# Kernel tuning notes

Measured on AMD Instinct MI355X. Metric: run time of the kernel, lower is better.

## Reference

```python
import jax, jax.numpy as jnp
import numpy as np
from math import sqrt

D_MODEL, N_H, D_H, D_CQ, D_CKV, D_HR = 2048, 16, 128, 768, 512, 64
B, S = 1, 2048


def _rope_cos_sin(seq_len, dim, base=10000.0):
    inv_freq = 1.0 / (base ** (jnp.arange(0, dim, 2, dtype=jnp.float32) / dim))
    ang = jnp.arange(seq_len, dtype=jnp.float32)[:, None] * inv_freq[None, :]  # (S, dim//2)
    return jnp.cos(ang), jnp.sin(ang)


def _rope(t, cos, sin):
    # t: (B, S, ..., dim) with sequence on axis 1; interleaved complex pairs
    shp = t.shape
    d2 = shp[-1] // 2
    tr = t.reshape(shp[:-1] + (d2, 2))
    x0, x1 = tr[..., 0], tr[..., 1]
    bshape = (1, shp[1]) + (1,) * (x0.ndim - 3) + (d2,)
    cs, sn = cos.reshape(bshape), sin.reshape(bshape)
    return jnp.stack([x0 * cs - x1 * sn, x0 * sn + x1 * cs], axis=-1).reshape(shp)


def setup_inputs() -> dict:
    key = jax.random.key(0)
    ks = jax.random.split(key, 10)
    sc = 0.02
    inp = {
        "x": jax.random.normal(ks[0], (B, S, D_MODEL), jnp.float32),
        "mask": jnp.triu(jnp.ones((S, S), dtype=bool), k=1),  # True -> masked (causal)
        "w_norm": jnp.ones((D_MODEL,), jnp.float32),
        "w_cq": jax.random.normal(ks[1], (D_MODEL, D_CQ), jnp.float32) * sc,
        "w_q": jax.random.normal(ks[2], (D_CQ, N_H * D_H), jnp.float32) * sc,
        "w_qr": jax.random.normal(ks[3], (D_CQ, N_H * D_HR), jnp.float32) * sc,
        "w_ckv": jax.random.normal(ks[4], (D_MODEL, D_CKV), jnp.float32) * sc,
        "w_k": jax.random.normal(ks[5], (D_CKV, N_H * D_H), jnp.float32) * sc,
        "w_kr": jax.random.normal(ks[6], (D_MODEL, D_HR), jnp.float32) * sc,
        "w_v": jax.random.normal(ks[7], (D_CKV, D_MODEL), jnp.float32) * sc,
        "w_o": jax.random.normal(ks[8], (N_H * D_H, D_MODEL), jnp.float32) * sc,
    }
    return inp


def reference(x, mask, w_norm, w_cq, w_q, w_qr, w_ckv, w_k, w_kr, w_v, w_o):
    b, s, _ = x.shape
    eps = jnp.finfo(x.dtype).eps
    h = x * jax.lax.rsqrt(jnp.mean(x * x, axis=-1, keepdims=True) + eps) * w_norm  # RMSNorm
    cos, sin = _rope_cos_sin(s, D_HR)

    c_q = h @ w_cq  # (b, s, d_c_q)
    q_c = (c_q @ w_q).reshape(b, s, N_H, D_H).transpose(0, 2, 1, 3)          # (b, h, s, d_h)
    q_r = _rope((c_q @ w_qr).reshape(b, s, N_H, D_HR), cos, sin).transpose(0, 2, 1, 3)
    q = jnp.concatenate([q_c, q_r], axis=-1)  # (b, h, s, d_h + d_h_R)

    c_kv = h @ w_ckv  # (b, s, d_c_kv)
    k_c = (c_kv @ w_k).reshape(b, s, N_H, D_H).transpose(0, 2, 1, 3)
    k_r = _rope(h @ w_kr, cos, sin)[:, None]  # (b, 1, s, d_h_R), shared across heads
    k = jnp.concatenate([k_c, jnp.broadcast_to(k_r, (b, N_H, s, D_HR))], axis=-1)
    v = (c_kv @ w_v).reshape(b, s, N_H, D_H).transpose(0, 2, 1, 3)

    score = jnp.einsum('bhqd,bhkd->bhqk', q, k) / sqrt(D_H + D_HR)
    score = jnp.where(mask, -jnp.inf, score)
    attn = jax.nn.softmax(score, axis=-1)
    out = jnp.einsum('bhqk,bhkd->bhqd', attn, v)  # (b, h, s, d_h)
    out = out.transpose(0, 2, 1, 3).reshape(b, s, N_H * D_H) @ w_o
    return x + out
```

## Files before the change

kernel.cpp:

```cpp
#include <hip/hip_runtime.h>
#include <hip/hip_bf16.h>
#include <math.h>

#define D_MODEL 2048
#define N_H     16
#define D_H     128
#define D_CQ    768
#define D_CKV   512
#define D_HR    64
#define SEQ     2048
#define N_ACT1  1408
#define NSPLIT  4

typedef short bf16x8 __attribute__((ext_vector_type(8)));
typedef float f32x4  __attribute__((ext_vector_type(4)));

__device__ inline short f2bf(float f) {
  union { float f; unsigned u; } v; v.f = f;
  unsigned r = (v.u + 0x7fff + ((v.u >> 16) & 1)) >> 16;
  return (short)r;
}
__device__ inline float bf2f(short s) {
  union { float f; unsigned u; } v; v.u = ((unsigned)(unsigned short)s) << 16;
  return v.f;
}

__device__ inline void gld_lds16(const void* g, void* l) {
#if __has_builtin(__builtin_amdgcn_global_load_lds)
  __builtin_amdgcn_global_load_lds(
      (const __attribute__((address_space(1))) unsigned int*)g,
      (__attribute__((address_space(3))) unsigned int*)l, 16, 0, 0);
#else
  int lane = threadIdx.x & 63;
  *((uint4*)l + lane) = *(const uint4*)g;
#endif
}

__global__ __launch_bounds__(256) void rmsnorm_kernel(
    const float* __restrict__ x, const float* __restrict__ w,
    short* __restrict__ hb) {
  int row = blockIdx.x;
  int tid = threadIdx.x;
  const float* xr = x + (size_t)row * D_MODEL;
  float ss = 0.f;
  for (int i = tid; i < D_MODEL; i += 256) { float v = xr[i]; ss += v * v; }
  __shared__ float red[256];
  red[tid] = ss;
  __syncthreads();
  for (int s = 128; s > 0; s >>= 1) {
    if (tid < s) red[tid] += red[tid + s];
    __syncthreads();
  }
  float scale = rsqrtf(red[0] / (float)D_MODEL + 1.1920929e-7f);
  short* hbr = hb + (size_t)row * D_MODEL;
  for (int i = tid; i < D_MODEL; i += 256) hbr[i] = f2bf(xr[i] * scale * w[i]);
}

struct CastJobs {
  const float* src[8];
  short* dst[8];
  int K[8];
  int pref[9];
  int nx[8];
};

__global__ __launch_bounds__(256) void cast_all(CastJobs J) {
  int bid = blockIdx.x;
  int j = 0;
#pragma unroll
  for (int t = 0; t < 8; t++)
    if (bid >= J.pref[t + 1]) j = t + 1;
  int lid = bid - J.pref[j];
  int nx = J.nx[j];
  int ty = lid / nx, tx = lid - ty * nx;
  int n0 = tx * 64, k0 = ty * 64;
  int K = J.K[j];
  const float* W = J.src[j];
  short* Wt = J.dst[j];
  int Nfull = nx * 64;

  __shared__ short T[64][68];
  int tid = threadIdx.x;
#pragma unroll
  for (int it = 0; it < 16; it++) {
    int idx = it * 256 + tid;
    int r = idx >> 6, c = idx & 63;
    T[c][r] = f2bf(W[(size_t)(k0 + r) * Nfull + n0 + c]);
  }
  __syncthreads();
#pragma unroll
  for (int it = 0; it < 16; it++) {
    int idx = it * 256 + tid;
    int r = idx >> 6, c = idx & 63;
    Wt[(size_t)(n0 + r) * K + k0 + c] = T[r][c];
  }
}

__device__ __forceinline__ void gemm64_body(
    const short* __restrict__ A, const short* __restrict__ Bt,
    float* __restrict__ Cf, short* __restrict__ Cb, short* __restrict__ Cb2,
    const float* __restrict__ addv, int M, int N, int K, int lda, int mode,
    int bxx, int byy) {
  __shared__ short As[64 * 64];
  __shared__ short Bs[128 * 64];
  int tid = threadIdx.x;
  int w = tid >> 6, l = tid & 63;
  int lq = l >> 4, l16 = l & 15;
  int bm = byy * 64, bn = bxx * 128;
  int wr = w >> 1, wc = w & 1;
  int wm0 = wr * 32, wn0 = wc * 64;

  f32x4 acc[2][4];
#pragma unroll
  for (int i = 0; i < 2; i++)
#pragma unroll
    for (int j = 0; j < 4; j++) acc[i][j] = (f32x4)0.f;

  int rsub = (l >> 3);
  int csub = ((l & 7) ^ rsub) << 3;

  for (int k0 = 0; k0 < K; k0 += 64) {
#pragma unroll
    for (int i = 0; i < 2; i++) {
      int r0 = i * 32 + w * 8;
      gld_lds16(A + (size_t)(bm + r0 + rsub) * lda + k0 + csub, As + r0 * 64);
    }
#pragma unroll
    for (int i = 0; i < 4; i++) {
      int r0 = i * 32 + w * 8;
      gld_lds16(Bt + (size_t)(bn + r0 + rsub) * K + k0 + csub, Bs + r0 * 64);
    }
    __syncthreads();

#pragma unroll
    for (int ks = 0; ks < 2; ks++) {
      bf16x8 af[2], bfr[4];
      int sw = ((ks * 4 + lq) ^ (l16 & 7)) << 3;
#pragma unroll
      for (int mt = 0; mt < 2; mt++)
        af[mt] = *(const bf16x8*)&As[(wm0 + mt * 16 + l16) * 64 + sw];
#pragma unroll
      for (int nt = 0; nt < 4; nt++)
        bfr[nt] = *(const bf16x8*)&Bs[(wn0 + nt * 16 + l16) * 64 + sw];
#pragma unroll
      for (int mt = 0; mt < 2; mt++)
#pragma unroll
        for (int nt = 0; nt < 4; nt++)
          acc[mt][nt] = __builtin_amdgcn_mfma_f32_16x16x32_bf16(af[mt], bfr[nt], acc[mt][nt], 0, 0, 0);
    }
    __syncthreads();
  }

#pragma unroll
  for (int mt = 0; mt < 2; mt++)
#pragma unroll
    for (int i = 0; i < 4; i++) {
      int row = bm + wm0 + mt * 16 + lq * 4 + i;
#pragma unroll
      for (int nt = 0; nt < 4; nt++) {
        int col = bn + wn0 + nt * 16 + l16;
        float v = acc[mt][nt][i];
        if (mode == 0) {
          size_t off = (size_t)row * N + col;
          if (addv) v += addv[off];
          Cf[off] = v;
        } else if (mode == 1) {
          Cb[(size_t)row * N + col] = f2bf(v);
        } else if (mode == 3) {
          if (col < 2048) {
            Cb[((size_t)(col >> 7) * M + row) * 192 + (col & 127)] = f2bf(v);
          } else {
            int cc = col - 2048;
            int hh = cc >> 6, dd = cc & 63;
            float partner = __shfl_xor(v, 1);
            float inv = __expf(-((float)(dd & ~1) / 64.0f) * 9.210340372f);
            float ang = (float)row * inv;
            float c = __cosf(ang), s = __sinf(ang);
            float res = ((dd & 1) == 0) ? (v * c - partner * s)
                                        : (partner * s + v * c);
            Cb[((size_t)hh * M + row) * 192 + 128 + dd] = f2bf(res);
          }
        } else {
          if (col < 2048) {
            Cb[((size_t)(col >> 7) * M + row) * 192 + (col & 127)] = f2bf(v);
          } else {
            Cb2[(size_t)row * D_MODEL + (col - 2048)] = f2bf(v);
          }
        }
      }
    }
}

__global__ __launch_bounds__(256) void gemm_bf16_64(
    const short* __restrict__ A, const short* __restrict__ Bt,
    float* __restrict__ Cf, short* __restrict__ Cb, short* __restrict__ Cb2,
    const float* __restrict__ addv, int M, int N, int K, int lda, int mode) {
  gemm64_body(A, Bt, Cf, Cb, Cb2, addv, M, N, K, lda, mode,
              blockIdx.x, blockIdx.y);
}

__global__ __launch_bounds__(256) void gemm_qkv(
    const short* __restrict__ act1, const short* __restrict__ WT2,
    const short* __restrict__ WT3, short* __restrict__ qb,
    short* __restrict__ kb, short* __restrict__ vb) {
  int bx = blockIdx.x;
  if (bx < 24) {
    gemm64_body(act1, WT2, nullptr, qb, nullptr, nullptr,
                SEQ, 3072, D_CQ, N_ACT1, 3, bx, blockIdx.y);
  } else {
    gemm64_body(act1 + 768, WT3, nullptr, kb, vb, nullptr,
                SEQ, 4096, D_CKV, N_ACT1, 4, bx - 24, blockIdx.y);
  }
}

__global__ void rope_k_kernel(const short* __restrict__ act1, short* __restrict__ kb) {
  int idx = blockIdx.x * blockDim.x + threadIdx.x;
  if (idx >= SEQ * 32) return;
  int j = idx & 31;
  int s = idx >> 5;
  const short* p = act1 + (size_t)s * N_ACT1 + 1280 + 2 * j;
  float x0 = bf2f(p[0]), x1 = bf2f(p[1]);
  float inv = __expf(-((float)(2 * j) / 64.0f) * 9.210340372f);
  float ang = (float)s * inv;
  float c = __cosf(ang), sn = __sinf(ang);
  short b0 = f2bf(x0 * c - x1 * sn);
  short b1 = f2bf(x0 * sn + x1 * c);
#pragma unroll
  for (int hh = 0; hh < N_H; hh++) {
    short* k = kb + ((size_t)hh * SEQ + s) * 192 + 128 + 2 * j;
    k[0] = b0;
    k[1] = b1;
  }
}

__global__ __launch_bounds__(256) void cast_v_t(
    const short* __restrict__ vb, short* __restrict__ vt) {
  int s0 = blockIdx.x * 64;
  int h = blockIdx.y;
  __shared__ short T[128][72];
  int tid = threadIdx.x;
#pragma unroll
  for (int it = 0; it < 32; it++) {
    int c = it * 256 + tid;
    int r = c >> 7, d = c & 127;
    T[d][r] = vb[(size_t)(s0 + r) * D_MODEL + h * 128 + d];
  }
  __syncthreads();
#pragma unroll
  for (int it = 0; it < 32; it++) {
    int c = it * 256 + tid;
    int d = c >> 6, s = c & 63;
    vt[(size_t)(h * 128 + d) * SEQ + s0 + s] = T[d][s];
  }
}

#define TQ 64
#define TK 64

__global__ __launch_bounds__(256) void attn_mfma(
    const short* __restrict__ qb, const short* __restrict__ kb,
    const short* __restrict__ vt, short* __restrict__ Opart,
    float* __restrict__ Lpart) {
  int bid = blockIdx.x;
  int h = bid & 15;
  int rest = bid >> 4;
  int qt = 31 - (rest / NSPLIT);
  int split = rest % NSPLIT;
  int q0 = qt * TQ;
  int nk = qt + 1;
  int tid = threadIdx.x;
  int wave = tid >> 6, lane = tid & 63;
  int lq = lane >> 4, l16 = lane & 15;

  __shared__ short Ks[TK * 192];
  __shared__ short Vs[128 * 64];
  __shared__ short Ps[TQ * 64];

  bf16x8 qf[6];
  {
    const short* qp = qb + ((size_t)h * SEQ + q0 + wave * 16 + l16) * 192;
#pragma unroll
    for (int ks = 0; ks < 6; ks++)
      qf[ks] = *(const bf16x8*)(qp + ks * 32 + lq * 8);
  }

  bf16x8 ones;
#pragma unroll
  for (int i = 0; i < 8; i++) ones[i] = (short)0x3F80;

  f32x4 O[8];
  f32x4 Ol = (f32x4)0.f;
#pragma unroll
  for (int i = 0; i < 8; i++) O[i] = (f32x4)0.f;
  const float scale = 0.07216878364870323f;

  int goffK[6];
#pragma unroll
  for (int i = 0; i < 6; i++) {
    int s = i * 256 + tid;
    int r = s / 24;
    int c = s - r * 24;
    goffK[i] = r * 192 + ((c ^ (r & 7)) << 3);
  }
  int goffV[4];
  int vrow[4];
#pragma unroll
  for (int i = 0; i < 4; i++) {
    int s = i * 256 + tid;
    int d = s >> 3;
    int p = s & 7;
    vrow[i] = d;
    goffV[i] = (p ^ (d & 7)) << 3;
  }
  const short* kb_h = kb + (size_t)h * SEQ * 192;
  const short* vt_h = vt + (size_t)h * 128 * SEQ;

  auto stage_k = [&](int k0s) {
#pragma unroll
    for (int i = 0; i < 6; i++)
      gld_lds16(kb_h + (size_t)k0s * 192 + goffK[i],
                Ks + (size_t)(i * 256 + wave * 64) * 8);
  };
  auto stage_v = [&](int k0s) {
#pragma unroll
    for (int i = 0; i < 4; i++)
      gld_lds16(vt_h + (size_t)vrow[i] * SEQ + k0s + goffV[i],
                Vs + (size_t)(i * 256 + wave * 64) * 8);
  };

  if (split < nk) stage_k(split * TK);

  for (int t = split; t < nk; t += NSPLIT) {
    int k0 = t * TK;
    __syncthreads();

    stage_v(k0);

    f32x4 S[4];
#pragma unroll
    for (int nt = 0; nt < 4; nt++) S[nt] = (f32x4)0.f;
#pragma unroll
    for (int ks = 0; ks < 6; ks++) {
#pragma unroll
      for (int nt = 0; nt < 4; nt++) {
        int row = nt * 16 + l16;
        bf16x8 b = *(const bf16x8*)&Ks[row * 192 +
                                       (((ks * 4 + lq) ^ (l16 & 7)) << 3)];
        S[nt] = __builtin_amdgcn_mfma_f32_16x16x32_bf16(qf[ks], b, S[nt], 0, 0, 0);
      }
    }

    bool diag = (k0 == q0);
#pragma unroll
    for (int i = 0; i < 4; i++) {
      int pr = wave * 16 + lq * 4 + i;
      int row = q0 + pr;
#pragma unroll
      for (int nt = 0; nt < 4; nt++) {
        float p;
        if (diag && (k0 + nt * 16 + l16 > row)) p = 0.f;
        else p = __expf(S[nt][i] * scale);
        int j = nt * 16 + l16;
        Ps[pr * 64 + ((((j >> 3) ^ (pr & 7)) << 3) | (j & 7))] = f2bf(p);
      }
    }

    __syncthreads();

    if (t + NSPLIT < nk) stage_k((t + NSPLIT) * TK);

#pragma unroll
    for (int kh = 0; kh < 2; kh++) {
      int prw = wave * 16 + l16;
      bf16x8 a = *(const bf16x8*)&Ps[prw * 64 +
                                     (((kh * 4 + lq) ^ (l16 & 7)) << 3)];
      Ol = __builtin_amdgcn_mfma_f32_16x16x32_bf16(a, ones, Ol, 0, 0, 0);
#pragma unroll
      for (int nt = 0; nt < 8; nt++) {
        int d = nt * 16 + l16;
        bf16x8 b = *(const bf16x8*)&Vs[d * 64 +
                                       (((kh * 4 + lq) ^ (d & 7)) << 3)];
        O[nt] = __builtin_amdgcn_mfma_f32_16x16x32_bf16(a, b, O[nt], 0, 0, 0);
      }
    }
  }

#pragma unroll
  for (int i = 0; i < 4; i++) {
    int row = q0 + wave * 16 + lq * 4 + i;
    size_t base = ((size_t)(split * N_H + h) * SEQ + row);
    size_t obase = base * 128;
#pragma unroll
    for (int nt = 0; nt < 8; nt++)
      Opart[obase + nt * 16 + l16] = f2bf(O[nt][i]);
    if (l16 == 0) Lpart[base] = Ol[i];
  }
}

__global__ __launch_bounds__(256) void attn_merge(
    const short* __restrict__ Opart, const float* __restrict__ Lpart,
    short* __restrict__ aob) {
  int q0 = blockIdx.x * 16;
  int h = blockIdx.y;
  int tid = threadIdx.x;
#pragma unroll
  for (int i = 0; i < 8; i++) {
    int c = i * 256 + tid;
    int row = q0 + (c >> 7), d = c & 127;
    float denom = 0.f, num = 0.f;
#pragma unroll
    for (int p = 0; p < NSPLIT; p++) {
      size_t base = (size_t)(p * N_H + h) * SEQ + row;
      denom += Lpart[base];
      num += bf2f(Opart[base * 128 + d]);
    }
    aob[(size_t)row * D_MODEL + h * 128 + d] = f2bf(num / denom);
  }
}

extern "C" void kernel_launch(void* const* d_in, const int* in_sizes, int n_in,
                              void* d_out, int out_size, void* d_ws, size_t ws_size,
                              hipStream_t stream) {
  const float* x      = (const float*)d_in[0];
  const float* w_norm = (const float*)d_in[2];
  const float* w_cq   = (const float*)d_in[3];
  const float* w_q    = (const float*)d_in[4];
  const float* w_qr   = (const float*)d_in[5];
  const float* w_ckv  = (const float*)d_in[6];
  const float* w_k    = (const float*)d_in[7];
  const float* w_kr   = (const float*)d_in[8];
  const float* w_v    = (const float*)d_in[9];
  const float* w_o    = (const float*)d_in[10];
  float* out = (float*)d_out;

  char* ws = (char*)d_ws;
  short* h_bf  = (short*)ws;  ws += (size_t)SEQ * D_MODEL * 2;
  short* act1  = (short*)ws;  ws += (size_t)SEQ * N_ACT1 * 2;
  short* qb    = (short*)ws;  ws += (size_t)N_H * SEQ * 192 * 2;
  short* kb    = (short*)ws;  ws += (size_t)N_H * SEQ * 192 * 2;
  short* vb    = (short*)ws;  ws += (size_t)SEQ * D_MODEL * 2;
  short* vt    = (short*)ws;  ws += (size_t)SEQ * D_MODEL * 2;
  short* ao_bf = (short*)ws;  ws += (size_t)SEQ * D_MODEL * 2;
  short* Opart = (short*)ws;  ws += (size_t)NSPLIT * N_H * SEQ * 128 * 2;
  float* Lpart = (float*)ws;  ws += (size_t)NSPLIT * N_H * SEQ * 4;
  short* WT1   = (short*)ws;  ws += (size_t)N_ACT1 * D_MODEL * 2;
  short* WT2   = (short*)ws;  ws += (size_t)3072 * D_CQ * 2;
  short* WT3   = (short*)ws;  ws += (size_t)4096 * D_CKV * 2;
  short* WTO   = (short*)ws;  ws += (size_t)D_MODEL * D_MODEL * 2;

  CastJobs J;
  J.src[0] = w_cq;  J.dst[0] = WT1;                              J.K[0] = D_MODEL; J.nx[0] = D_CQ / 64;
  J.src[1] = w_ckv; J.dst[1] = WT1 + (size_t)768 * D_MODEL;      J.K[1] = D_MODEL; J.nx[1] = D_CKV / 64;
  J.src[2] = w_kr;  J.dst[2] = WT1 + (size_t)1280 * D_MODEL;     J.K[2] = D_MODEL; J.nx[2] = D_HR / 64;
  J.src[3] = w_q;   J.dst[3] = WT2;                              J.K[3] = D_CQ;    J.nx[3] = 2048 / 64;
  J.src[4] = w_qr;  J.dst[4] = WT2 + (size_t)2048 * D_CQ;        J.K[4] = D_CQ;    J.nx[4] = 1024 / 64;
  J.src[5] = w_k;   J.dst[5] = WT3;                              J.K[5] = D_CKV;   J.nx[5] = 2048 / 64;
  J.src[6] = w_v;   J.dst[6] = WT3 + (size_t)2048 * D_CKV;       J.K[6] = D_CKV;   J.nx[6] = 2048 / 64;
  J.src[7] = w_o;   J.dst[7] = WTO;                              J.K[7] = D_MODEL; J.nx[7] = 2048 / 64;
  int pref = 0;
  for (int j = 0; j < 8; j++) {
    J.pref[j] = pref;
    pref += J.nx[j] * (J.K[j] / 64);
  }
  J.pref[8] = pref;
  cast_all<<<pref, 256, 0, stream>>>(J);

  rmsnorm_kernel<<<SEQ, 256, 0, stream>>>(x, w_norm, h_bf);

  gemm_bf16_64<<<dim3(N_ACT1 / 128, SEQ / 64), 256, 0, stream>>>(
      h_bf, WT1, nullptr, act1, nullptr, nullptr, SEQ, N_ACT1, D_MODEL, D_MODEL, 1);

  rope_k_kernel<<<(SEQ * 32 + 255) / 256, 256, 0, stream>>>(act1, kb);

  gemm_qkv<<<dim3(24 + 32, SEQ / 64), 256, 0, stream>>>(
      act1, WT2, WT3, qb, kb, vb);

  cast_v_t<<<dim3(SEQ / 64, N_H), 256, 0, stream>>>(vb, vt);

  attn_mfma<<<dim3(32 * NSPLIT * N_H), 256, 0, stream>>>(qb, kb, vt, Opart, Lpart);
  attn_merge<<<dim3(SEQ / 16, N_H), 256, 0, stream>>>(Opart, Lpart, ao_bf);

  gemm_bf16_64<<<dim3(D_MODEL / 128, SEQ / 64), 256, 0, stream>>>(
      ao_bf, WTO, out, nullptr, nullptr, x, SEQ, D_MODEL, D_MODEL, D_MODEL, 0);
}
```

Measured before the change: 303.3 us.

## Double query tile per attention block so each K/V tile feeds two row-tiles

Result: no change. 301.3 us (-0.7%).

```diff
diff --git a/kernel.cpp b/kernel.cpp
--- a/kernel.cpp
+++ b/kernel.cpp
@@ -254,20 +254,20 @@
   }
 }
 
-#define TQ 64
+#define TQ 128
 #define TK 64
 
-__global__ __launch_bounds__(256) void attn_mfma(
+__global__ __launch_bounds__(256, 2) void attn_mfma(
     const short* __restrict__ qb, const short* __restrict__ kb,
     const short* __restrict__ vt, short* __restrict__ Opart,
     float* __restrict__ Lpart) {
   int bid = blockIdx.x;
   int h = bid & 15;
   int rest = bid >> 4;
-  int qt = 31 - (rest / NSPLIT);
+  int qt = 15 - (rest / NSPLIT);
   int split = rest % NSPLIT;
   int q0 = qt * TQ;
-  int nk = qt + 1;
+  int nk = 2 * (qt + 1);
   int tid = threadIdx.x;
   int wave = tid >> 6, lane = tid & 63;
   int lq = lane >> 4, l16 = lane & 15;
@@ -276,22 +276,28 @@
   __shared__ short Vs[128 * 64];
   __shared__ short Ps[TQ * 64];
 
-  bf16x8 qf[6];
+  bf16x8 qf[2][6];
   {
-    const short* qp = qb + ((size_t)h * SEQ + q0 + wave * 16 + l16) * 192;
-#pragma unroll
-    for (int ks = 0; ks < 6; ks++)
-      qf[ks] = *(const bf16x8*)(qp + ks * 32 + lq * 8);
+    const short* qp = qb + ((size_t)h * SEQ + q0 + wave * 32 + l16) * 192;
+#pragma unroll
+    for (int mt = 0; mt < 2; mt++)
+#pragma unroll
+      for (int ks = 0; ks < 6; ks++)
+        qf[mt][ks] = *(const bf16x8*)(qp + (size_t)mt * 16 * 192 + ks * 32 + lq * 8);
   }
 
   bf16x8 ones;
 #pragma unroll
   for (int i = 0; i < 8; i++) ones[i] = (short)0x3F80;
 
-  f32x4 O[8];
-  f32x4 Ol = (f32x4)0.f;
-#pragma unroll
-  for (int i = 0; i < 8; i++) O[i] = (f32x4)0.f;
+  f32x4 O[2][8];
+  f32x4 Ol[2];
+#pragma unroll
+  for (int mt = 0; mt < 2; mt++) {
+    Ol[mt] = (f32x4)0.f;
+#pragma unroll
+    for (int i = 0; i < 8; i++) O[mt][i] = (f32x4)0.f;
+  }
   const float scale = 0.07216878364870323f;
 
   int goffK[6];
@@ -336,9 +342,12 @@
 
     stage_v(k0);
 
-    f32x4 S[4];
-#pragma unroll
-    for (int nt = 0; nt < 4; nt++) S[nt] = (f32x4)0.f;
+    f32x4 S[2][4];
+#pragma unroll
+    for (int mt = 0; mt < 2; mt++)
+#pragma unroll
+      for (int nt = 0; nt < 4; nt++) S[mt][nt] = (f32x4)0.f;
+    __builtin_amdgcn_s_setprio(1);
 #pragma unroll
     for (int ks = 0; ks < 6; ks++) {
 #pragma unroll
@@ -346,55 +355,70 @@
         int row = nt * 16 + l16;
         bf16x8 b = *(const bf16x8*)&Ks[row * 192 +
                                        (((ks * 4 + lq) ^ (l16 & 7)) << 3)];
-        S[nt] = __builtin_amdgcn_mfma_f32_16x16x32_bf16(qf[ks], b, S[nt], 0, 0, 0);
+#pragma unroll
+        for (int mt = 0; mt < 2; mt++)
+          S[mt][nt] = __builtin_amdgcn_mfma_f32_16x16x32_bf16(qf[mt][ks], b, S[mt][nt], 0, 0, 0);
       }
     }
-
-    bool diag = (k0 == q0);
-#pragma unroll
-    for (int i = 0; i < 4; i++) {
-      int pr = wave * 16 + lq * 4 + i;
-      int row = q0 + pr;
-#pragma unroll
-      for (int nt = 0; nt < 4; nt++) {
-        float p;
-        if (diag && (k0 + nt * 16 + l16 > row)) p = 0.f;
-        else p = __expf(S[nt][i] * scale);
-        int j = nt * 16 + l16;
-        Ps[pr * 64 + ((((j >> 3) ^ (pr & 7)) << 3) | (j & 7))] = f2bf(p);
+    __builtin_amdgcn_s_setprio(0);
+
+#pragma unroll
+    for (int mt = 0; mt < 2; mt++)
+#pragma unroll
+      for (int i = 0; i < 4; i++) {
+        int pr = wave * 32 + mt * 16 + lq * 4 + i;
+        int row = q0 + pr;
+        bool may = (k0 + 63 > row);
+#pragma unroll
+        for (int nt = 0; nt < 4; nt++) {
+          float p;
+          if (may && (k0 + nt * 16 + l16 > row)) p = 0.f;
+          else p = __expf(S[mt][nt][i] * scale);
+          int j = nt * 16 + l16;
+          Ps[pr * 64 + ((((j >> 3) ^ (pr & 7)) << 3) | (j & 7))] = f2bf(p);
+        }
       }
-    }
 
     __syncthreads();
 
     if (t + NSPLIT < nk) stage_k((t + NSPLIT) * TK);
 
+    __builtin_amdgcn_s_setprio(1);
 #pragma unroll
     for (int kh = 0; kh < 2; kh++) {
-      int prw = wave * 16 + l16;
-      bf16x8 a = *(const bf16x8*)&Ps[prw * 64 +
-                                     (((kh * 4 + lq) ^ (l16 & 7)) << 3)];
-      Ol = __builtin_amdgcn_mfma_f32_16x16x32_bf16(a, ones, Ol, 0, 0, 0);
+      bf16x8 a[2];
+#pragma unroll
+      for (int mt = 0; mt < 2; mt++) {
+        int prw = wave * 32 + mt * 16 + l16;
+        a[mt] = *(const bf16x8*)&Ps[prw * 64 +
+                                    (((kh * 4 + lq) ^ (l16 & 7)) << 3)];
+        Ol[mt] = __builtin_amdgcn_mfma_f32_16x16x32_bf16(a[mt], ones, Ol[mt], 0, 0, 0);
+      }
 #pragma unroll
       for (int nt = 0; nt < 8; nt++) {
         int d = nt * 16 + l16;
         bf16x8 b = *(const bf16x8*)&Vs[d * 64 +
                                        (((kh * 4 + lq) ^ (d & 7)) << 3)];
-        O[nt] = __builtin_amdgcn_mfma_f32_16x16x32_bf16(a, b, O[nt], 0, 0, 0);
+#pragma unroll
+        for (int mt = 0; mt < 2; mt++)
+          O[mt][nt] = __builtin_amdgcn_mfma_f32_16x16x32_bf16(a[mt], b, O[mt][nt], 0, 0, 0);
       }
     }
-  }
-
-#pragma unroll
-  for (int i = 0; i < 4; i++) {
-    int row = q0 + wave * 16 + lq * 4 + i;
-    size_t base = ((size_t)(split * N_H + h) * SEQ + row);
-    size_t obase = base * 128;
-#pragma unroll
-    for (int nt = 0; nt < 8; nt++)
-      Opart[obase + nt * 16 + l16] = f2bf(O[nt][i]);
-    if (l16 == 0) Lpart[base] = Ol[i];
-  }
+    __builtin_amdgcn_s_setprio(0);
+  }
+
+#pragma unroll
+  for (int mt = 0; mt < 2; mt++)
+#pragma unroll
+    for (int i = 0; i < 4; i++) {
+      int row = q0 + wave * 32 + mt * 16 + lq * 4 + i;
+      size_t base = ((size_t)(split * N_H + h) * SEQ + row);
+      size_t obase = base * 128;
+#pragma unroll
+      for (int nt = 0; nt < 8; nt++)
+        Opart[obase + nt * 16 + l16] = f2bf(O[mt][nt][i]);
+      if (l16 == 0) Lpart[base] = Ol[mt][i];
+    }
 }
 
 __global__ __launch_bounds__(256) void attn_merge(
@@ -477,7 +501,7 @@
 
   cast_v_t<<<dim3(SEQ / 64, N_H), 256, 0, stream>>>(vb, vt);
 
-  attn_mfma<<<dim3(32 * NSPLIT * N_H), 256, 0, stream>>>(qb, kb, vt, Opart, Lpart);
+  attn_mfma<<<dim3((SEQ / TQ) * NSPLIT * N_H), 256, 0, stream>>>(qb, kb, vt, Opart, Lpart);
   attn_merge<<<dim3(SEQ / 16, N_H), 256, 0, stream>>>(Opart, Lpart, ao_bf);
 
   gemm_bf16_64<<<dim3(D_MODEL / 128, SEQ / 64), 256, 0, stream>>>(
```
